# Kernel tuning notes

Hardware: AMD Instinct MI355X
Metric: run time of the kernel (lower is better)

Reference implementation:

```python
import jax, jax.numpy as jnp
import numpy as np

B = 256      # number of graphs (args.batch_size)
NPG = 1000   # nodes per graph (args.num_node)
C = 64       # in_channels
DEG = 16     # avg degree
K = 500      # ceil(ratio * NPG), ratio = 0.5
EPS = 1e-8


def setup_inputs() -> dict:
    key = jax.random.key(0)
    k1, k2, k3, k4, k5 = jax.random.split(key, 5)
    N = B * NPG
    epg = NPG * DEG  # edges per graph
    x = jax.random.normal(k1, (N, C), jnp.float32)
    src = jax.random.randint(k2, (B, epg), 0, NPG)
    dst = jax.random.randint(k3, (B, epg), 0, NPG)
    off = (jnp.arange(B, dtype=jnp.int32) * NPG)[:, None]
    edge_index = jnp.stack([(src + off).reshape(-1), (dst + off).reshape(-1)]).astype(jnp.int32)
    edge_attr = jax.random.uniform(k4, (B * epg,), jnp.float32)
    batch = jnp.repeat(jnp.arange(B, dtype=jnp.int32), NPG)
    W = jax.random.normal(k5, (C, C), jnp.float32) * (1.0 / np.sqrt(C))
    b = jnp.zeros((C,), jnp.float32)
    return {"istraining": 1, "x": x, "edge_index": edge_index, "edge_attr": edge_attr,
            "batch": batch, "W": W, "b": b}


def _gcn_conv(x, edge_index, W, b):
    # PyG GCNConv: x' = D^{-1/2} (A + I) D^{-1/2} X W + b, unit edge weights.
    N = x.shape[0]
    sl = jnp.arange(N, dtype=edge_index.dtype)
    src = jnp.concatenate([edge_index[0], sl])  # message source j
    dst = jnp.concatenate([edge_index[1], sl])  # aggregation target i
    deg = jnp.zeros((N,), x.dtype).at[dst].add(1.0)
    dinv = jnp.where(deg > 0, jax.lax.rsqrt(jnp.maximum(deg, 1.0)), 0.0)
    norm = dinv[src] * dinv[dst]          # [E+N]
    h = x @ W                              # [N, C]
    msg = h[src] * norm[:, None]           # gather + scale (dominant traffic)
    out = jax.ops.segment_sum(msg, dst, num_segments=N) + b
    return out


def _node_score(x):
    # compute_node_score: cosine similarity of each node to its graph centroid
    # (community prototype), plus KL(softmax(score) || uniform) per graph.
    xb = x.reshape(B, NPG, C)
    cen = xb.mean(axis=1, keepdims=True)                       # [B,1,C]
    num = jnp.sum(xb * cen, axis=-1)                           # [B,NPG]
    den = jnp.linalg.norm(xb, axis=-1) * jnp.linalg.norm(cen, axis=-1) + EPS
    score = num / den                                          # [B,NPG]
    logp = jax.nn.log_softmax(score, axis=1)
    kl = jnp.sum(jnp.exp(logp) * (logp + jnp.log(jnp.float32(NPG))), axis=1)  # [B]
    indices_ = jnp.argsort(-score, axis=1)                     # [B,NPG]
    return score, kl, indices_


def reference(istraining, x, edge_index, edge_attr, batch, W, b):
    N = x.shape[0]
    x = _gcn_conv(x, edge_index, W, b)
    score, kl_all_batch, indices_ = _node_score(x)
    # per-graph top-k (fixed k since every graph has NPG nodes)
    _, idx = jax.lax.top_k(score, K)                           # [B,K]
    perm = ((jnp.arange(B, dtype=idx.dtype) * NPG)[:, None] + idx).reshape(-1)  # [B*K]
    score_flat = score.reshape(-1)
    x_new = x[perm] * jnp.tanh(score_flat[perm])[:, None]
    batch_new = batch[perm]
    # filter_adj: keep edges with both endpoints retained, re-index to new ids.
    mapping = jnp.full((N,), -1, dtype=jnp.int32).at[perm].set(
        jnp.arange(perm.shape[0], dtype=jnp.int32))
    new_ei = mapping[edge_index]                               # [2,E], -1 = dropped
    edge_mask = jnp.logical_and(new_ei[0] >= 0, new_ei[1] >= 0)
    edge_attr_new = jnp.where(edge_mask, edge_attr, 0.0)
    return (x_new, new_ei, edge_attr_new, edge_mask, batch_new, perm, kl_all_batch, indices_)
```

## Files before the change

### kernel.cpp

```cpp
#include <hip/hip_runtime.h>
#include <math.h>

#define NPG 1000
#define KTOP 500
#define C 64
#define EPG 16000

__device__ __forceinline__ float readlane_f(float v, int l) {
    return __uint_as_float(__builtin_amdgcn_readlane(__float_as_uint(v), (unsigned)l));
}
__device__ __forceinline__ int readlane_i(int v, int l) {
    return (int)__builtin_amdgcn_readlane((unsigned)v, (unsigned)l);
}

__global__ __launch_bounds__(256) void build_graph_k(const int* __restrict__ ei, int E,
                                                     int* __restrict__ deg,
                                                     float* __restrict__ dinv,
                                                     int* __restrict__ off,
                                                     int* __restrict__ csr) {
    int g = blockIdx.x, t = threadIdx.x;
    __shared__ int cnt[NPG];
    __shared__ int soff[NPG];
    __shared__ unsigned short lcsr[EPG];
    __shared__ int red[256];
    const int gbase = g * NPG;
    const int ebase = g * EPG;
    const int* __restrict__ srcp = ei + ebase;
    const int* __restrict__ dstp = ei + E + ebase;

    for (int i = t; i < NPG; i += 256) cnt[i] = 0;
    __syncthreads();
    for (int i = t; i < EPG; i += 256) atomicAdd(&cnt[dstp[i] - gbase], 1);
    __syncthreads();
    int base = t * 4;
    int v0 = 0, v1 = 0, v2 = 0, v3 = 0;
    if (base + 0 < NPG) v0 = cnt[base + 0];
    if (base + 1 < NPG) v1 = cnt[base + 1];
    if (base + 2 < NPG) v2 = cnt[base + 2];
    if (base + 3 < NPG) v3 = cnt[base + 3];
    int s = v0 + v1 + v2 + v3;
    red[t] = s;
    __syncthreads();
    for (int o = 1; o < 256; o <<= 1) {
        int xx = (t >= o) ? red[t - o] : 0;
        __syncthreads();
        red[t] += xx;
        __syncthreads();
    }
    int p = red[t] - s;
    if (base + 0 < NPG) { soff[base + 0] = p; p += v0; }
    if (base + 1 < NPG) { soff[base + 1] = p; p += v1; }
    if (base + 2 < NPG) { soff[base + 2] = p; p += v2; }
    if (base + 3 < NPG) { soff[base + 3] = p; p += v3; }
    __syncthreads();
    for (int i = t; i < NPG; i += 256) {
        int d = cnt[i];
        deg[gbase + i] = d;
        dinv[gbase + i] = 1.0f / sqrtf((float)(d + 1));
        off[gbase + i] = ebase + soff[i];
    }
    __syncthreads();
    for (int i = t; i < NPG; i += 256) cnt[i] = soff[i];
    __syncthreads();
    for (int i = t; i < EPG; i += 256) {
        int d = dstp[i] - gbase;
        int pos = atomicAdd(&cnt[d], 1);
        lcsr[pos] = (unsigned short)(srcp[i] - gbase);
    }
    __syncthreads();
    int4* co = (int4*)(csr + ebase);
    for (int i = t; i < EPG / 4; i += 256) {
        int4 v;
        v.x = gbase + (int)lcsr[i * 4 + 0];
        v.y = gbase + (int)lcsr[i * 4 + 1];
        v.z = gbase + (int)lcsr[i * 4 + 2];
        v.w = gbase + (int)lcsr[i * 4 + 3];
        co[i] = v;
    }
}

__global__ __launch_bounds__(256) void gemm_k(const float* __restrict__ x,
                                              const float* __restrict__ W,
                                              const float* __restrict__ dinv,
                                              float* __restrict__ h2, int N) {
    __shared__ float sW[C * C];
    int t = threadIdx.x;
    for (int i = t; i < C * C / 4; i += 256) ((float4*)sW)[i] = ((const float4*)W)[i];
    __syncthreads();
    int r0 = blockIdx.x * 512 + t;
    int r1 = r0 + 256;
    if (r0 >= N) return;
    bool has1 = (r1 < N);
    const float4* x0 = (const float4*)(x + (size_t)r0 * C);
    const float4* x1 = (const float4*)(x + (size_t)(has1 ? r1 : r0) * C);
    float acc0[C], acc1[C];
#pragma unroll
    for (int i = 0; i < C; ++i) { acc0[i] = 0.f; acc1[i] = 0.f; }
    float4 a0 = x0[0], a1 = x1[0];
    for (int k4 = 0; k4 < 16; ++k4) {
        float4 b0, b1;
        if (k4 < 15) { b0 = x0[k4 + 1]; b1 = x1[k4 + 1]; }
        const float4* wr = (const float4*)(sW + k4 * 4 * C);
        const float* a0f = (const float*)&a0;
        const float* a1f = (const float*)&a1;
#pragma unroll
        for (int c4 = 0; c4 < 16; ++c4) {
            float4 w[4];
            w[0] = wr[c4]; w[1] = wr[16 + c4]; w[2] = wr[32 + c4]; w[3] = wr[48 + c4];
            const float* wf = (const float*)w;
#pragma unroll
            for (int j = 0; j < 4; ++j) {
                float s0 = acc0[c4 * 4 + j], s1 = acc1[c4 * 4 + j];
#pragma unroll
                for (int kk = 0; kk < 4; ++kk) {
                    float wv = wf[kk * 4 + j];
                    s0 = fmaf(a0f[kk], wv, s0);
                    s1 = fmaf(a1f[kk], wv, s1);
                }
                acc0[c4 * 4 + j] = s0; acc1[c4 * 4 + j] = s1;
            }
        }
        a0 = b0; a1 = b1;
    }
    float dv0 = dinv[r0];
    float dv1 = has1 ? dinv[r1] : 0.f;
#pragma unroll
    for (int i = 0; i < C; ++i) { acc0[i] *= dv0; acc1[i] *= dv1; }
    float4* h0 = (float4*)(h2 + (size_t)r0 * C);
#pragma unroll
    for (int q = 0; q < 16; ++q) h0[q] = ((float4*)acc0)[q];
    if (has1) {
        float4* h1 = (float4*)(h2 + (size_t)r1 * C);
#pragma unroll
        for (int q = 0; q < 16; ++q) h1[q] = ((float4*)acc1)[q];
    }
}

__global__ __launch_bounds__(256) void gather_k(const int* __restrict__ csr,
                                                const int* __restrict__ off,
                                                const int* __restrict__ deg,
                                                const float* __restrict__ h2,
                                                const float* __restrict__ dinv,
                                                const float* __restrict__ bias,
                                                float* __restrict__ out2, int N, int B) {
    int b = blockIdx.x;
    int wave = threadIdx.x >> 6;
    int lane = threadIdx.x & 63;
    int node;
    if ((B & 7) == 0) {
        int xcd = b & 7, slot = b >> 3;
        int gpx = B >> 3;
        int g = xcd * gpx + slot / (NPG / 4);
        int blkin = slot % (NPG / 4);
        node = g * NPG + blkin * 4 + wave;
    } else {
        node = b * 4 + wave;
    }
    if (node >= N) return;
    int o0 = off[node], dg = deg[node];
    float di = dinv[node];
    float hv2 = h2[(size_t)node * C + lane];
    int sv = 0;
    if (lane < dg) sv = csr[o0 + lane];
    float acc = 0.f;
    int jmax = dg < 64 ? dg : 64;
    int j = 0;
    for (; j + 8 <= jmax; j += 8) {
        int s0 = readlane_i(sv, j + 0);
        int s1 = readlane_i(sv, j + 1);
        int s2 = readlane_i(sv, j + 2);
        int s3 = readlane_i(sv, j + 3);
        int s4 = readlane_i(sv, j + 4);
        int s5 = readlane_i(sv, j + 5);
        int s6 = readlane_i(sv, j + 6);
        int s7 = readlane_i(sv, j + 7);
        float v0 = h2[(size_t)s0 * C + lane];
        float v1 = h2[(size_t)s1 * C + lane];
        float v2 = h2[(size_t)s2 * C + lane];
        float v3 = h2[(size_t)s3 * C + lane];
        float v4 = h2[(size_t)s4 * C + lane];
        float v5 = h2[(size_t)s5 * C + lane];
        float v6 = h2[(size_t)s6 * C + lane];
        float v7 = h2[(size_t)s7 * C + lane];
        acc += ((v0 + v1) + (v2 + v3)) + ((v4 + v5) + (v6 + v7));
    }
    for (; j + 4 <= jmax; j += 4) {
        int s0 = readlane_i(sv, j + 0);
        int s1 = readlane_i(sv, j + 1);
        int s2 = readlane_i(sv, j + 2);
        int s3 = readlane_i(sv, j + 3);
        float v0 = h2[(size_t)s0 * C + lane];
        float v1 = h2[(size_t)s1 * C + lane];
        float v2 = h2[(size_t)s2 * C + lane];
        float v3 = h2[(size_t)s3 * C + lane];
        acc += (v0 + v1) + (v2 + v3);
    }
    for (; j < jmax; ++j) {
        int s = readlane_i(sv, j);
        acc += h2[(size_t)s * C + lane];
    }
    for (; j < dg; ++j) {
        int s = csr[o0 + j];
        acc += h2[(size_t)s * C + lane];
    }
    out2[(size_t)node * C + lane] = bias[lane] + di * (acc + hv2);
}

__global__ void centroid_part_k(const float* __restrict__ out2, float* __restrict__ pcen) {
    int blk = blockIdx.x;
    int g = blk >> 2, p = blk & 3;
    int t = threadIdx.x;
    int c = t & 63, q = t >> 6;
    const float* base = out2 + (size_t)g * NPG * C;
    int n0 = p * 250, n1 = n0 + 250;
    float acc = 0.f;
    for (int n = n0 + q; n < n1; n += 4) acc += base[(size_t)n * C + c];
    __shared__ float red[256];
    red[t] = acc;
    __syncthreads();
    if (t < 64) pcen[(size_t)blk * C + t] = red[t] + red[64 + t] + red[128 + t] + red[192 + t];
}

__global__ void cen_fin_k(const float* __restrict__ pcen, float* __restrict__ cen,
                          float* __restrict__ cnorm) {
    int g = blockIdx.x, c = threadIdx.x;
    float s = pcen[(size_t)(g * 4 + 0) * C + c] + pcen[(size_t)(g * 4 + 1) * C + c]
            + pcen[(size_t)(g * 4 + 2) * C + c] + pcen[(size_t)(g * 4 + 3) * C + c];
    float m = s / 1000.0f;
    cen[g * C + c] = m;
    float v = m * m;
    for (int o = 32; o > 0; o >>= 1) v += __shfl_down(v, o, 64);
    if (c == 0) cnorm[g] = sqrtf(v);
}

__global__ void score_k(const float* __restrict__ out2, const float* __restrict__ cen,
                        const float* __restrict__ cnorm, float* __restrict__ score, int N) {
    int i = blockIdx.x * 256 + threadIdx.x;
    if (i < N) {
        int g = i / NPG;
        const float4* xr = (const float4*)(out2 + (size_t)i * C);
        const float4* cr = (const float4*)(cen + g * C);
        float num = 0.f, sq = 0.f;
#pragma unroll
        for (int q = 0; q < 16; ++q) {
            float4 a = xr[q], b = cr[q];
            num += a.x * b.x + a.y * b.y + a.z * b.z + a.w * b.w;
            sq  += a.x * a.x + a.y * a.y + a.z * a.z + a.w * a.w;
        }
        float den = sqrtf(sq) * cnorm[g] + 1e-8f;
        score[i] = num / den;
    }
}

__global__ void softmax_kl_k(const float* __restrict__ score, float* __restrict__ o_kl) {
    int g = blockIdx.x, t = threadIdx.x;
    __shared__ float ss[NPG];
    __shared__ float red[256];
    const float4* s4 = (const float4*)(score + (size_t)g * NPG);
    for (int i = t; i < NPG / 4; i += 256) ((float4*)ss)[i] = s4[i];
    __syncthreads();
    float mx = -INFINITY;
    for (int i = t; i < NPG; i += 256) mx = fmaxf(mx, ss[i]);
    red[t] = mx;
    __syncthreads();
    for (int w = 128; w > 0; w >>= 1) { if (t < w) red[t] = fmaxf(red[t], red[t + w]); __syncthreads(); }
    mx = red[0];
    __syncthreads();
    float se = 0.f;
    for (int i = t; i < NPG; i += 256) se += expf(ss[i] - mx);
    red[t] = se;
    __syncthreads();
    for (int w = 128; w > 0; w >>= 1) { if (t < w) red[t] += red[t + w]; __syncthreads(); }
    float lse = logf(red[0]);
    __syncthreads();
    float kl = 0.f;
    const float ln_npg = 6.9077552790f;
    for (int i = t; i < NPG; i += 256) {
        float lp = ss[i] - mx - lse;
        kl += expf(lp) * (lp + ln_npg);
    }
    red[t] = kl;
    __syncthreads();
    for (int w = 128; w > 0; w >>= 1) { if (t < w) red[t] += red[t + w]; __syncthreads(); }
    if (t == 0) o_kl[g] = red[0];
}

__global__ void sort_k(const float* __restrict__ score, int* __restrict__ sidx,
                       float* __restrict__ o_ind) {
    __shared__ unsigned long long kk[1024];
    int g = blockIdx.x, t = threadIdx.x;
    for (int i = t; i < 1024; i += 512) {
        unsigned long long v;
        if (i < NPG) {
            unsigned u = __float_as_uint(score[(size_t)g * NPG + i]);
            u = (u & 0x80000000u) ? ~u : (u | 0x80000000u);
            v = ((unsigned long long)(~u) << 32) | (unsigned)i;
        } else {
            v = ~0ULL;
        }
        kk[i] = v;
    }
    __syncthreads();
    for (int k = 2; k <= 1024; k <<= 1) {
        for (int j = k >> 1; j > 0; j >>= 1) {
            for (int i = t; i < 1024; i += 512) {
                int ixj = i ^ j;
                if (ixj > i) {
                    unsigned long long a = kk[i], b = kk[ixj];
                    bool up = ((i & k) == 0);
                    if ((a > b) == up) { kk[i] = b; kk[ixj] = a; }
                }
            }
            __syncthreads();
        }
    }
    for (int i = t; i < NPG; i += 512) {
        int idx = (int)(kk[i] & 0xFFFFFFFFULL);
        sidx[(size_t)g * NPG + i] = idx;
        o_ind[(size_t)g * NPG + i] = (float)idx;
    }
}

__global__ void topk_k(const int* __restrict__ sidx, const float* __restrict__ score,
                       const float* __restrict__ out2, int* __restrict__ mapping,
                       float* __restrict__ o_xnew, float* __restrict__ o_batch,
                       float* __restrict__ o_perm, int BK) {
    int j = blockIdx.x * 256 + threadIdx.x;
    if (j < BK) {
        int b = j / KTOP, r = j - b * KTOP;
        int node = sidx[(size_t)b * NPG + r];
        int gn = b * NPG + node;
        mapping[gn] = j;
        o_perm[j] = (float)gn;
        o_batch[j] = (float)b;
        float tn = tanhf(score[gn]);
        const float4* src = (const float4*)(out2 + (size_t)gn * C);
        float4* dst = (float4*)(o_xnew + (size_t)j * C);
#pragma unroll
        for (int q = 0; q < 16; ++q) {
            float4 v = src[q];
            v.x *= tn; v.y *= tn; v.z *= tn; v.w *= tn;
            dst[q] = v;
        }
    }
}

__global__ void edge_out_k(const int* __restrict__ ei, const float* __restrict__ eattr,
                           const int* __restrict__ mapping, float* __restrict__ o_newei,
                           float* __restrict__ o_eattr, float* __restrict__ o_mask, int E) {
    int e4 = blockIdx.x * 256 + threadIdx.x;
    int q = E >> 2;
    if (e4 < q) {
        int4 sidx = ((const int4*)ei)[e4];
        int4 didx = ((const int4*)ei)[q + e4];
        int a0 = mapping[sidx.x], a1 = mapping[sidx.y], a2 = mapping[sidx.z], a3 = mapping[sidx.w];
        int b0 = mapping[didx.x], b1 = mapping[didx.y], b2 = mapping[didx.z], b3 = mapping[didx.w];
        float4 f0 = { (float)a0, (float)a1, (float)a2, (float)a3 };
        float4 f1 = { (float)b0, (float)b1, (float)b2, (float)b3 };
        ((float4*)o_newei)[e4] = f0;
        ((float4*)o_newei)[q + e4] = f1;
        float4 at = ((const float4*)eattr)[e4];
        float4 mk, ea;
        mk.x = (a0 >= 0 && b0 >= 0) ? 1.0f : 0.0f;
        mk.y = (a1 >= 0 && b1 >= 0) ? 1.0f : 0.0f;
        mk.z = (a2 >= 0 && b2 >= 0) ? 1.0f : 0.0f;
        mk.w = (a3 >= 0 && b3 >= 0) ? 1.0f : 0.0f;
        ea.x = mk.x != 0.0f ? at.x : 0.0f;
        ea.y = mk.y != 0.0f ? at.y : 0.0f;
        ea.z = mk.z != 0.0f ? at.z : 0.0f;
        ea.w = mk.w != 0.0f ? at.w : 0.0f;
        ((float4*)o_mask)[e4] = mk;
        ((float4*)o_eattr)[e4] = ea;
    }
}

extern "C" void kernel_launch(void* const* d_in, const int* in_sizes, int n_in,
                              void* d_out, int out_size, void* d_ws, size_t ws_size,
                              hipStream_t stream) {
    (void)n_in; (void)out_size; (void)ws_size;
    const float* x     = (const float*)d_in[1];
    const int*   ei    = (const int*)d_in[2];
    const float* eattr = (const float*)d_in[3];
    const float* W     = (const float*)d_in[5];
    const float* bias  = (const float*)d_in[6];

    const int N  = in_sizes[1] / C;
    const int E  = in_sizes[2] / 2;
    const int B  = N / NPG;
    const int BK = B * KTOP;

    char* wsp = (char*)d_ws;
    float* out2    = (float*)wsp; wsp += (size_t)N * C * 4;
    float* dinv    = (float*)wsp; wsp += (size_t)N * 4;
    float* score   = (float*)wsp; wsp += (size_t)N * 4;
    float* cen     = (float*)wsp; wsp += (size_t)B * C * 4;
    float* cnorm   = (float*)wsp; wsp += 1024;
    int*   sidx    = (int*)wsp;   wsp += (size_t)B * NPG * 4;
    int*   mapping = (int*)wsp;   wsp += (size_t)N * 4;
    int*   deg     = (int*)wsp;   wsp += (size_t)N * 4;
    int*   off     = (int*)wsp;   wsp += (size_t)N * 4;
    float* pcen    = (float*)wsp; wsp += (size_t)B * 4 * C * 4;

    float* out     = (float*)d_out;
    float* o_xnew  = out;
    float* o_newei = o_xnew + (size_t)BK * C;
    float* o_eattr = o_newei + 2 * (size_t)E;
    float* o_mask  = o_eattr + (size_t)E;
    float* o_batch = o_mask + (size_t)E;
    float* o_perm  = o_batch + (size_t)BK;
    float* o_kl    = o_perm + (size_t)BK;
    float* o_ind   = o_kl + (size_t)B;

    float* h2buf = out;
    int*   csr   = (int*)o_eattr;

    hipMemsetAsync(mapping, 0xFF, (size_t)N * 4, stream);

    build_graph_k<<<B, 256, 0, stream>>>(ei, E, deg, dinv, off, csr);
    gemm_k<<<(N + 511) / 512, 256, 0, stream>>>(x, W, dinv, h2buf, N);
    gather_k<<<(N + 3) / 4, 256, 0, stream>>>(csr, off, deg, h2buf, dinv, bias, out2, N, B);
    centroid_part_k<<<B * 4, 256, 0, stream>>>(out2, pcen);
    cen_fin_k<<<B, 64, 0, stream>>>(pcen, cen, cnorm);
    score_k<<<(N + 255) / 256, 256, 0, stream>>>(out2, cen, cnorm, score, N);
    softmax_kl_k<<<B, 256, 0, stream>>>(score, o_kl);
    sort_k<<<B, 512, 0, stream>>>(score, sidx, o_ind);
    topk_k<<<(BK + 255) / 256, 256, 0, stream>>>(sidx, score, out2, mapping,
                                                 o_xnew, o_batch, o_perm, BK);
    edge_out_k<<<(E / 4 + 255) / 256, 256, 0, stream>>>(ei, eattr, mapping,
                                                        o_newei, o_eattr, o_mask, E);
}
```

Baseline: 491.7 us.

## Fuse centroid reduction into gather, process four nodes per wave, widen sort/build blocks

```diff
diff --git a/kernel.cpp b/kernel.cpp
--- a/kernel.cpp
+++ b/kernel.cpp
@@ -5,6 +5,7 @@
 #define KTOP 500
 #define C 64
 #define EPG 16000
+#define BPG 63
 
 __device__ __forceinline__ float readlane_f(float v, int l) {
     return __uint_as_float(__builtin_amdgcn_readlane(__float_as_uint(v), (unsigned)l));
@@ -13,69 +14,59 @@
     return (int)__builtin_amdgcn_readlane((unsigned)v, (unsigned)l);
 }
 
-__global__ __launch_bounds__(256) void build_graph_k(const int* __restrict__ ei, int E,
-                                                     int* __restrict__ deg,
-                                                     float* __restrict__ dinv,
-                                                     int* __restrict__ off,
-                                                     int* __restrict__ csr) {
+__global__ __launch_bounds__(1024) void build_graph_k(const int* __restrict__ ei, int E,
+                                                      int* __restrict__ deg,
+                                                      float* __restrict__ dinv,
+                                                      int* __restrict__ off,
+                                                      int* __restrict__ csr) {
     int g = blockIdx.x, t = threadIdx.x;
     __shared__ int cnt[NPG];
     __shared__ int soff[NPG];
     __shared__ unsigned short lcsr[EPG];
-    __shared__ int red[256];
+    __shared__ int red[1024];
     const int gbase = g * NPG;
     const int ebase = g * EPG;
     const int* __restrict__ srcp = ei + ebase;
     const int* __restrict__ dstp = ei + E + ebase;
 
-    for (int i = t; i < NPG; i += 256) cnt[i] = 0;
-    __syncthreads();
-    for (int i = t; i < EPG; i += 256) atomicAdd(&cnt[dstp[i] - gbase], 1);
-    __syncthreads();
-    int base = t * 4;
-    int v0 = 0, v1 = 0, v2 = 0, v3 = 0;
-    if (base + 0 < NPG) v0 = cnt[base + 0];
-    if (base + 1 < NPG) v1 = cnt[base + 1];
-    if (base + 2 < NPG) v2 = cnt[base + 2];
-    if (base + 3 < NPG) v3 = cnt[base + 3];
-    int s = v0 + v1 + v2 + v3;
-    red[t] = s;
-    __syncthreads();
-    for (int o = 1; o < 256; o <<= 1) {
+    for (int i = t; i < NPG; i += 1024) cnt[i] = 0;
+    __syncthreads();
+    for (int i = t; i < EPG; i += 1024) atomicAdd(&cnt[dstp[i] - gbase], 1);
+    __syncthreads();
+    int v = (t < NPG) ? cnt[t] : 0;
+    red[t] = v;
+    __syncthreads();
+    for (int o = 1; o < 1024; o <<= 1) {
         int xx = (t >= o) ? red[t - o] : 0;
         __syncthreads();
         red[t] += xx;
         __syncthreads();
     }
-    int p = red[t] - s;
-    if (base + 0 < NPG) { soff[base + 0] = p; p += v0; }
-    if (base + 1 < NPG) { soff[base + 1] = p; p += v1; }
-    if (base + 2 < NPG) { soff[base + 2] = p; p += v2; }
-    if (base + 3 < NPG) { soff[base + 3] = p; p += v3; }
-    __syncthreads();
-    for (int i = t; i < NPG; i += 256) {
+    if (t < NPG) soff[t] = red[t] - v;
+    __syncthreads();
+    for (int i = t; i < NPG; i += 1024) {
         int d = cnt[i];
         deg[gbase + i] = d;
         dinv[gbase + i] = 1.0f / sqrtf((float)(d + 1));
         off[gbase + i] = ebase + soff[i];
     }
     __syncthreads();
-    for (int i = t; i < NPG; i += 256) cnt[i] = soff[i];
-    __syncthreads();
-    for (int i = t; i < EPG; i += 256) {
+    for (int i = t; i < NPG; i += 1024) cnt[i] = soff[i];
+    __syncthreads();
+    for (int i = t; i < EPG; i += 1024) {
         int d = dstp[i] - gbase;
         int pos = atomicAdd(&cnt[d], 1);
         lcsr[pos] = (unsigned short)(srcp[i] - gbase);
     }
     __syncthreads();
     int4* co = (int4*)(csr + ebase);
-    for (int i = t; i < EPG / 4; i += 256) {
-        int4 v;
-        v.x = gbase + (int)lcsr[i * 4 + 0];
-        v.y = gbase + (int)lcsr[i * 4 + 1];
-        v.z = gbase + (int)lcsr[i * 4 + 2];
-        v.w = gbase + (int)lcsr[i * 4 + 3];
-        co[i] = v;
+    for (int i = t; i < EPG / 4; i += 1024) {
+        int4 vv;
+        vv.x = gbase + (int)lcsr[i * 4 + 0];
+        vv.y = gbase + (int)lcsr[i * 4 + 1];
+        vv.z = gbase + (int)lcsr[i * 4 + 2];
+        vv.w = gbase + (int)lcsr[i * 4 + 3];
+        co[i] = vv;
     }
 }
 
@@ -142,91 +133,111 @@
                                                 const float* __restrict__ h2,
                                                 const float* __restrict__ dinv,
                                                 const float* __restrict__ bias,
-                                                float* __restrict__ out2, int N, int B) {
-    int b = blockIdx.x;
+                                                float* __restrict__ out2,
+                                                float* __restrict__ cen_sum,
+                                                int N, int B) {
+    __shared__ float cenacc[C];
+    int blk = blockIdx.x;
     int wave = threadIdx.x >> 6;
     int lane = threadIdx.x & 63;
-    int node;
+    int t = threadIdx.x;
+    int g, blkin;
     if ((B & 7) == 0) {
-        int xcd = b & 7, slot = b >> 3;
-        int gpx = B >> 3;
-        int g = xcd * gpx + slot / (NPG / 4);
-        int blkin = slot % (NPG / 4);
-        node = g * NPG + blkin * 4 + wave;
+        int xcd = blk & 7, slot = blk >> 3;
+        g = (slot / BPG) * 8 + xcd;
+        blkin = slot % BPG;
     } else {
-        node = b * 4 + wave;
-    }
-    if (node >= N) return;
-    int o0 = off[node], dg = deg[node];
-    float di = dinv[node];
-    float hv2 = h2[(size_t)node * C + lane];
-    int sv = 0;
-    if (lane < dg) sv = csr[o0 + lane];
-    float acc = 0.f;
-    int jmax = dg < 64 ? dg : 64;
-    int j = 0;
-    for (; j + 8 <= jmax; j += 8) {
-        int s0 = readlane_i(sv, j + 0);
-        int s1 = readlane_i(sv, j + 1);
-        int s2 = readlane_i(sv, j + 2);
-        int s3 = readlane_i(sv, j + 3);
-        int s4 = readlane_i(sv, j + 4);
-        int s5 = readlane_i(sv, j + 5);
-        int s6 = readlane_i(sv, j + 6);
-        int s7 = readlane_i(sv, j + 7);
-        float v0 = h2[(size_t)s0 * C + lane];
-        float v1 = h2[(size_t)s1 * C + lane];
-        float v2 = h2[(size_t)s2 * C + lane];
-        float v3 = h2[(size_t)s3 * C + lane];
-        float v4 = h2[(size_t)s4 * C + lane];
-        float v5 = h2[(size_t)s5 * C + lane];
-        float v6 = h2[(size_t)s6 * C + lane];
-        float v7 = h2[(size_t)s7 * C + lane];
-        acc += ((v0 + v1) + (v2 + v3)) + ((v4 + v5) + (v6 + v7));
-    }
-    for (; j + 4 <= jmax; j += 4) {
-        int s0 = readlane_i(sv, j + 0);
-        int s1 = readlane_i(sv, j + 1);
-        int s2 = readlane_i(sv, j + 2);
-        int s3 = readlane_i(sv, j + 3);
-        float v0 = h2[(size_t)s0 * C + lane];
-        float v1 = h2[(size_t)s1 * C + lane];
-        float v2 = h2[(size_t)s2 * C + lane];
-        float v3 = h2[(size_t)s3 * C + lane];
-        acc += (v0 + v1) + (v2 + v3);
-    }
-    for (; j < jmax; ++j) {
-        int s = readlane_i(sv, j);
-        acc += h2[(size_t)s * C + lane];
-    }
-    for (; j < dg; ++j) {
-        int s = csr[o0 + j];
-        acc += h2[(size_t)s * C + lane];
-    }
-    out2[(size_t)node * C + lane] = bias[lane] + di * (acc + hv2);
-}
-
-__global__ void centroid_part_k(const float* __restrict__ out2, float* __restrict__ pcen) {
-    int blk = blockIdx.x;
-    int g = blk >> 2, p = blk & 3;
-    int t = threadIdx.x;
-    int c = t & 63, q = t >> 6;
-    const float* base = out2 + (size_t)g * NPG * C;
-    int n0 = p * 250, n1 = n0 + 250;
-    float acc = 0.f;
-    for (int n = n0 + q; n < n1; n += 4) acc += base[(size_t)n * C + c];
-    __shared__ float red[256];
-    red[t] = acc;
-    __syncthreads();
-    if (t < 64) pcen[(size_t)blk * C + t] = red[t] + red[64 + t] + red[128 + t] + red[192 + t];
-}
-
-__global__ void cen_fin_k(const float* __restrict__ pcen, float* __restrict__ cen,
+        g = blk / BPG;
+        blkin = blk % BPG;
+    }
+    if (t < C) cenacc[t] = 0.f;
+    __syncthreads();
+
+    int base = blkin * 4 + wave;
+    bool active = (base < NPG / 4);
+    float csum = 0.f;
+    if (active) {
+        int nA = g * NPG + base;
+        int nB = nA + 250, nC = nA + 500, nD = nA + 750;
+        int oA = off[nA], oB = off[nB], oC = off[nC], oD = off[nD];
+        int dA = deg[nA], dB = deg[nB], dC = deg[nC], dD = deg[nD];
+        float diA = dinv[nA], diB = dinv[nB], diC = dinv[nC], diD = dinv[nD];
+        float hA = h2[(size_t)nA * C + lane];
+        float hB = h2[(size_t)nB * C + lane];
+        float hC = h2[(size_t)nC * C + lane];
+        float hD = h2[(size_t)nD * C + lane];
+        float bv = bias[lane];
+        int svA = (lane < dA) ? csr[oA + lane] : nA;
+        int svB = (lane < dB) ? csr[oB + lane] : nB;
+        int svC = (lane < dC) ? csr[oC + lane] : nC;
+        int svD = (lane < dD) ? csr[oD + lane] : nD;
+        int jmA = dA < 64 ? dA : 64;
+        int jmB = dB < 64 ? dB : 64;
+        int jmC = dC < 64 ? dC : 64;
+        int jmD = dD < 64 ? dD : 64;
+        int rA = (jmA + 3) & ~3, rB = (jmB + 3) & ~3;
+        int rC = (jmC + 3) & ~3, rD = (jmD + 3) & ~3;
+        int m0 = rA > rB ? rA : rB;
+        int m1 = rC > rD ? rC : rD;
+        int mmax = m0 > m1 ? m0 : m1;
+        float aA = 0.f, aB = 0.f, aC = 0.f, aD = 0.f;
+        for (int j = 0; j < mmax; j += 4) {
+            int sA0 = readlane_i(svA, j + 0), sA1 = readlane_i(svA, j + 1);
+            int sA2 = readlane_i(svA, j + 2), sA3 = readlane_i(svA, j + 3);
+            int sB0 = readlane_i(svB, j + 0), sB1 = readlane_i(svB, j + 1);
+            int sB2 = readlane_i(svB, j + 2), sB3 = readlane_i(svB, j + 3);
+            int sC0 = readlane_i(svC, j + 0), sC1 = readlane_i(svC, j + 1);
+            int sC2 = readlane_i(svC, j + 2), sC3 = readlane_i(svC, j + 3);
+            int sD0 = readlane_i(svD, j + 0), sD1 = readlane_i(svD, j + 1);
+            int sD2 = readlane_i(svD, j + 2), sD3 = readlane_i(svD, j + 3);
+            float vA0 = h2[(size_t)sA0 * C + lane];
+            float vA1 = h2[(size_t)sA1 * C + lane];
+            float vA2 = h2[(size_t)sA2 * C + lane];
+            float vA3 = h2[(size_t)sA3 * C + lane];
+            float vB0 = h2[(size_t)sB0 * C + lane];
+            float vB1 = h2[(size_t)sB1 * C + lane];
+            float vB2 = h2[(size_t)sB2 * C + lane];
+            float vB3 = h2[(size_t)sB3 * C + lane];
+            float vC0 = h2[(size_t)sC0 * C + lane];
+            float vC1 = h2[(size_t)sC1 * C + lane];
+            float vC2 = h2[(size_t)sC2 * C + lane];
+            float vC3 = h2[(size_t)sC3 * C + lane];
+            float vD0 = h2[(size_t)sD0 * C + lane];
+            float vD1 = h2[(size_t)sD1 * C + lane];
+            float vD2 = h2[(size_t)sD2 * C + lane];
+            float vD3 = h2[(size_t)sD3 * C + lane];
+            aA += (vA0 + vA1) + (vA2 + vA3);
+            aB += (vB0 + vB1) + (vB2 + vB3);
+            aC += (vC0 + vC1) + (vC2 + vC3);
+            aD += (vD0 + vD1) + (vD2 + vD3);
+        }
+        for (int j = 64; j < dA; ++j) aA += h2[(size_t)csr[oA + j] * C + lane];
+        for (int j = 64; j < dB; ++j) aB += h2[(size_t)csr[oB + j] * C + lane];
+        for (int j = 64; j < dC; ++j) aC += h2[(size_t)csr[oC + j] * C + lane];
+        for (int j = 64; j < dD; ++j) aD += h2[(size_t)csr[oD + j] * C + lane];
+        float cA = 1.0f - (float)(mmax - jmA);
+        float cB = 1.0f - (float)(mmax - jmB);
+        float cC = 1.0f - (float)(mmax - jmC);
+        float cD = 1.0f - (float)(mmax - jmD);
+        float resA = fmaf(diA, fmaf(cA, hA, aA), bv);
+        float resB = fmaf(diB, fmaf(cB, hB, aB), bv);
+        float resC = fmaf(diC, fmaf(cC, hC, aC), bv);
+        float resD = fmaf(diD, fmaf(cD, hD, aD), bv);
+        out2[(size_t)nA * C + lane] = resA;
+        out2[(size_t)nB * C + lane] = resB;
+        out2[(size_t)nC * C + lane] = resC;
+        out2[(size_t)nD * C + lane] = resD;
+        csum = (resA + resB) + (resC + resD);
+        atomicAdd(&cenacc[lane], csum);
+    }
+    __syncthreads();
+    if (t < C) atomicAdd(&cen_sum[(size_t)g * C + t], cenacc[t]);
+}
+
+__global__ void cen_fin_k(const float* __restrict__ cen_sum, float* __restrict__ cen,
                           float* __restrict__ cnorm) {
     int g = blockIdx.x, c = threadIdx.x;
-    float s = pcen[(size_t)(g * 4 + 0) * C + c] + pcen[(size_t)(g * 4 + 1) * C + c]
-            + pcen[(size_t)(g * 4 + 2) * C + c] + pcen[(size_t)(g * 4 + 3) * C + c];
-    float m = s / 1000.0f;
+    float m = cen_sum[(size_t)g * C + c] / 1000.0f;
     cen[g * C + c] = m;
     float v = m * m;
     for (int o = 32; o > 0; o >>= 1) v += __shfl_down(v, o, 64);
@@ -285,39 +296,36 @@
     if (t == 0) o_kl[g] = red[0];
 }
 
-__global__ void sort_k(const float* __restrict__ score, int* __restrict__ sidx,
-                       float* __restrict__ o_ind) {
+__global__ __launch_bounds__(1024) void sort_k(const float* __restrict__ score,
+                                               int* __restrict__ sidx,
+                                               float* __restrict__ o_ind) {
     __shared__ unsigned long long kk[1024];
     int g = blockIdx.x, t = threadIdx.x;
-    for (int i = t; i < 1024; i += 512) {
-        unsigned long long v;
-        if (i < NPG) {
-            unsigned u = __float_as_uint(score[(size_t)g * NPG + i]);
-            u = (u & 0x80000000u) ? ~u : (u | 0x80000000u);
-            v = ((unsigned long long)(~u) << 32) | (unsigned)i;
-        } else {
-            v = ~0ULL;
-        }
-        kk[i] = v;
-    }
+    unsigned long long v;
+    if (t < NPG) {
+        unsigned u = __float_as_uint(score[(size_t)g * NPG + t]);
+        u = (u & 0x80000000u) ? ~u : (u | 0x80000000u);
+        v = ((unsigned long long)(~u) << 32) | (unsigned)t;
+    } else {
+        v = ~0ULL;
+    }
+    kk[t] = v;
     __syncthreads();
     for (int k = 2; k <= 1024; k <<= 1) {
         for (int j = k >> 1; j > 0; j >>= 1) {
-            for (int i = t; i < 1024; i += 512) {
-                int ixj = i ^ j;
-                if (ixj > i) {
-                    unsigned long long a = kk[i], b = kk[ixj];
-                    bool up = ((i & k) == 0);
-                    if ((a > b) == up) { kk[i] = b; kk[ixj] = a; }
-                }
+            int ixj = t ^ j;
+            if (ixj > t) {
+                unsigned long long a = kk[t], b = kk[ixj];
+                bool up = ((t & k) == 0);
+                if ((a > b) == up) { kk[t] = b; kk[ixj] = a; }
             }
             __syncthreads();
         }
     }
-    for (int i = t; i < NPG; i += 512) {
-        int idx = (int)(kk[i] & 0xFFFFFFFFULL);
-        sidx[(size_t)g * NPG + i] = idx;
-        o_ind[(size_t)g * NPG + i] = (float)idx;
+    if (t < NPG) {
+        int idx = (int)(kk[t] & 0xFFFFFFFFULL);
+        sidx[(size_t)g * NPG + t] = idx;
+        o_ind[(size_t)g * NPG + t] = (float)idx;
     }
 }
 
@@ -399,7 +407,7 @@
     int*   mapping = (int*)wsp;   wsp += (size_t)N * 4;
     int*   deg     = (int*)wsp;   wsp += (size_t)N * 4;
     int*   off     = (int*)wsp;   wsp += (size_t)N * 4;
-    float* pcen    = (float*)wsp; wsp += (size_t)B * 4 * C * 4;
+    float* cen_sum = (float*)wsp; wsp += (size_t)B * C * 4;
 
     float* out     = (float*)d_out;
     float* o_xnew  = out;
@@ -415,15 +423,16 @@
     int*   csr   = (int*)o_eattr;
 
     hipMemsetAsync(mapping, 0xFF, (size_t)N * 4, stream);
-
-    build_graph_k<<<B, 256, 0, stream>>>(ei, E, deg, dinv, off, csr);
+    hipMemsetAsync(cen_sum, 0, (size_t)B * C * 4, stream);
+
+    build_graph_k<<<B, 1024, 0, stream>>>(ei, E, deg, dinv, off, csr);
     gemm_k<<<(N + 511) / 512, 256, 0, stream>>>(x, W, dinv, h2buf, N);
-    gather_k<<<(N + 3) / 4, 256, 0, stream>>>(csr, off, deg, h2buf, dinv, bias, out2, N, B);
-    centroid_part_k<<<B * 4, 256, 0, stream>>>(out2, pcen);
-    cen_fin_k<<<B, 64, 0, stream>>>(pcen, cen, cnorm);
+    gather_k<<<B * BPG, 256, 0, stream>>>(csr, off, deg, h2buf, dinv, bias, out2,
+                                          cen_sum, N, B);
+    cen_fin_k<<<B, 64, 0, stream>>>(cen_sum, cen, cnorm);
     score_k<<<(N + 255) / 256, 256, 0, stream>>>(out2, cen, cnorm, score, N);
     softmax_kl_k<<<B, 256, 0, stream>>>(score, o_kl);
-    sort_k<<<B, 512, 0, stream>>>(score, sidx, o_ind);
+    sort_k<<<B, 1024, 0, stream>>>(score, sidx, o_ind);
     topk_k<<<(BK + 255) / 256, 256, 0, stream>>>(sidx, score, out2, mapping,
                                                  o_xnew, o_batch, o_perm, BK);
     edge_out_k<<<(E / 4 + 255) / 256, 256, 0, stream>>>(ei, eattr, mapping,
```

New measurement: 397.9 us. 1.24x faster.
